# Kernel tuning notes

Hardware: AMD Instinct MI355X
Metric: run time of the kernel (lower is better)

## Reference

```python
import jax, jax.numpy as jnp
import numpy as np

EPS = 1e-6
N_HEADS = 16


def _stable_softmax(x):
    # max subtracted with stop_gradient (torch .detach()), clamp to [-50, 50], eps in denom
    x_max = jax.lax.stop_gradient(jnp.max(x, axis=-1, keepdims=True))
    exp_x = jnp.exp(jnp.clip(x - x_max, -50.0, 50.0))
    return exp_x / (jnp.sum(exp_x, axis=-1, keepdims=True) + EPS)


def setup_inputs() -> dict:
    key = jax.random.key(0)
    k1, k2, k3 = jax.random.split(key, 3)
    B, S, D = 2, 2048, 1024
    x = jax.random.normal(k1, (B, S, D), dtype=jnp.float32)
    Wqkv = jax.random.normal(k2, (3 * D, D), dtype=jnp.float32) * 0.02
    Wout = jax.random.normal(k3, (D, D), dtype=jnp.float32) * (0.02 / np.sqrt(2))
    return {"x": x, "Wqkv": Wqkv, "Wout": Wout}


def reference(x, Wqkv, Wout):
    B, S, D = x.shape
    H = N_HEADS
    Dh = D // H
    scale = 1.0 / np.sqrt(Dh)
    # qkv projection (torch Linear: x @ W.T), split into q,k,v -> (B,H,S,Dh)
    qkv = (x @ Wqkv.T).reshape(B, S, 3, H, Dh)
    qkv = jnp.transpose(qkv, (2, 0, 3, 1, 4))
    q, k, v = qkv[0], qkv[1], qkv[2]
    # chunked attention is mathematically identical to full attention here
    scores = jnp.einsum('bhqd,bhkd->bhqk', q, k) * scale
    attn = _stable_softmax(scores)
    out = jnp.einsum('bhqk,bhkd->bhqd', attn, v)  # (B,H,S,Dh)
    out = jnp.transpose(out, (0, 2, 1, 3)).reshape(B, S, D)
    return out @ Wout.T
```

## Files before the change

### kernel.cpp

```cpp
#include <hip/hip_runtime.h>
#include <hip/hip_bf16.h>
#include <stdint.h>

#define S_LEN   2048
#define D_MODEL 1024
#define NH      16
#define DH      64
#define BATCH   2
#define TOKENS  (BATCH * S_LEN)

typedef __bf16 bf16;
typedef __bf16 bf16x8 __attribute__((ext_vector_type(8)));
typedef __bf16 b16x4  __attribute__((ext_vector_type(4)));
typedef float  f32x4  __attribute__((ext_vector_type(4)));
typedef float  f32x16 __attribute__((ext_vector_type(16)));
typedef unsigned int uint32;

__device__ __forceinline__ void async_lds16(const void* g, void* l) {
  __builtin_amdgcn_global_load_lds((__attribute__((address_space(1))) void*)g,
                                   (__attribute__((address_space(3))) void*)l,
                                   16, 0, 0);
}

#define MFMA16(a, b, c) __builtin_amdgcn_mfma_f32_16x16x32_bf16((a), (b), (c), 0, 0, 0)

__global__ __launch_bounds__(256) void convert2_kernel(
    const float* __restrict__ s0, bf16* __restrict__ d0, int n0,
    const float* __restrict__ s1, bf16* __restrict__ d1, int n1) {
  int i = blockIdx.x * 256 + threadIdx.x;
  const float* s;
  bf16* d;
  if (i < n0) {
    s = s0 + (size_t)i * 8; d = d0 + (size_t)i * 8;
  } else {
    i -= n0;
    if (i >= n1) return;
    s = s1 + (size_t)i * 8; d = d1 + (size_t)i * 8;
  }
  const f32x4 a = *(const f32x4*)s;
  const f32x4 b = *(const f32x4*)(s + 4);
  bf16x8 o;
#pragma unroll
  for (int j = 0; j < 4; j++) { o[j] = (bf16)a[j]; o[j + 4] = (bf16)b[j]; }
  *(bf16x8*)d = o;
}

__global__ __launch_bounds__(512, 2) void gemm_qkv_kernel(
    const bf16* __restrict__ X, const bf16* __restrict__ W,
    bf16* __restrict__ Qo, bf16* __restrict__ Ko, bf16* __restrict__ VTo) {
  extern __shared__ __align__(16) bf16 smem[];
  bf16* const Asb = smem;
  bf16* const Bsb = smem + 32768;

  const int tid  = threadIdx.x;
  const int wave = tid >> 6, lane = tid & 63;
  const int quad = lane >> 4, l16 = lane & 15;
  const int wm = (wave >> 2) * 128;
  const int wn = (wave & 3) * 64;
  const int m0 = blockIdx.y * 256;
  const int n0 = blockIdx.x * 256;

  const int rowc  = tid >> 3;
  const int koffc = ((tid & 7) ^ (rowc & 7)) * 8;
  const bf16* pAlo = X + (size_t)(m0 + rowc) * D_MODEL + koffc;
  const bf16* pAhi = X + (size_t)(m0 + 128 + rowc) * D_MODEL + koffc;
  const bf16* pBlo = W + (size_t)(n0 + rowc) * D_MODEL + koffc;
  const bf16* pBhi = W + (size_t)(n0 + 128 + rowc) * D_MODEL + koffc;
  const int ldc = tid * 8;

  const int swr = l16 & 7;
  const int ko0 = ((0 + quad) ^ swr) * 8;
  const int ko1 = ((4 + quad) ^ swr) * 8;

  f32x4 acc[8][4] = {};
  bf16x8 af[4][2], bfr[4][2];

#define STG(P, LB)                                                        \
  { async_lds16((P), (LB) + ldc);                                         \
    async_lds16((P) + (size_t)64 * D_MODEL, (LB) + ldc + 4096); }

#define BAR()                                                             \
  { asm volatile("" ::: "memory");                                        \
    __builtin_amdgcn_s_barrier();                                         \
    asm volatile("" ::: "memory"); }

  STG(pAlo, Asb)                 pAlo += 64;
  STG(pAhi, Asb + 8192)          pAhi += 64;
  STG(pBlo, Bsb)                 pBlo += 64;
  STG(pBhi, Bsb + 8192)          pBhi += 64;
  STG(pAlo, Asb + 16384)         pAlo += 64;
  STG(pAhi, Asb + 16384 + 8192)  pAhi += 64;
  asm volatile("s_waitcnt vmcnt(4)" ::: "memory");
  __builtin_amdgcn_s_barrier();

#pragma unroll 2
  for (int t = 0; t < 16; t++) {
    const int cur = t & 1;
    const bf16* Ac = Asb + cur * 16384;
    const bf16* Bc = Bsb + cur * 16384;
    bf16* An = Asb + cur * 16384;
    bf16* Bn = Bsb + (cur ^ 1) * 16384;

#pragma unroll
    for (int i = 0; i < 4; i++) {
      af[i][0] = *(const bf16x8*)(Ac + (wm + i * 16 + l16) * 64 + ko0);
      af[i][1] = *(const bf16x8*)(Ac + (wm + i * 16 + l16) * 64 + ko1);
    }
#pragma unroll
    for (int j = 0; j < 2; j++) {
      bfr[j][0] = *(const bf16x8*)(Bc + (wn + j * 16 + l16) * 64 + ko0);
      bfr[j][1] = *(const bf16x8*)(Bc + (wn + j * 16 + l16) * 64 + ko1);
    }
    if (t < 15) { STG(pBlo, Bn) pBlo += 64; }
    BAR();
    __builtin_amdgcn_s_setprio(1);
#pragma unroll
    for (int i = 0; i < 4; i++)
#pragma unroll
      for (int j = 0; j < 2; j++) {
        acc[i][j] = MFMA16(af[i][0], bfr[j][0], acc[i][j]);
        acc[i][j] = MFMA16(af[i][1], bfr[j][1], acc[i][j]);
      }
    __builtin_amdgcn_s_setprio(0);
    BAR();

#pragma unroll
    for (int j = 2; j < 4; j++) {
      bfr[j][0] = *(const bf16x8*)(Bc + (wn + j * 16 + l16) * 64 + ko0);
      bfr[j][1] = *(const bf16x8*)(Bc + (wn + j * 16 + l16) * 64 + ko1);
    }
    if (t < 15) { STG(pBhi, Bn + 8192) pBhi += 64; }
    BAR();
    __builtin_amdgcn_s_setprio(1);
#pragma unroll
    for (int i = 0; i < 4; i++)
#pragma unroll
      for (int j = 2; j < 4; j++) {
        acc[i][j] = MFMA16(af[i][0], bfr[j][0], acc[i][j]);
        acc[i][j] = MFMA16(af[i][1], bfr[j][1], acc[i][j]);
      }
    __builtin_amdgcn_s_setprio(0);
    BAR();

#pragma unroll
    for (int i = 0; i < 4; i++) {
      af[i][0] = *(const bf16x8*)(Ac + (wm + (i + 4) * 16 + l16) * 64 + ko0);
      af[i][1] = *(const bf16x8*)(Ac + (wm + (i + 4) * 16 + l16) * 64 + ko1);
    }
    if (t < 14) { STG(pAlo, An) pAlo += 64; }
    BAR();
    __builtin_amdgcn_s_setprio(1);
#pragma unroll
    for (int i = 0; i < 4; i++)
#pragma unroll
      for (int j = 0; j < 2; j++) {
        acc[i + 4][j] = MFMA16(af[i][0], bfr[j][0], acc[i + 4][j]);
        acc[i + 4][j] = MFMA16(af[i][1], bfr[j][1], acc[i + 4][j]);
      }
    __builtin_amdgcn_s_setprio(0);
    BAR();

    if (t < 14) {
      STG(pAhi, An + 8192) pAhi += 64;
      asm volatile("s_waitcnt vmcnt(4)" ::: "memory");
    } else if (t == 14) {
      asm volatile("s_waitcnt vmcnt(0)" ::: "memory");
    }
    BAR();
    __builtin_amdgcn_s_setprio(1);
#pragma unroll
    for (int i = 0; i < 4; i++)
#pragma unroll
      for (int j = 2; j < 4; j++) {
        acc[i + 4][j] = MFMA16(af[i][0], bfr[j][0], acc[i + 4][j]);
        acc[i + 4][j] = MFMA16(af[i][1], bfr[j][1], acc[i + 4][j]);
      }
    __builtin_amdgcn_s_setprio(0);
    BAR();
  }
#undef STG
#undef BAR

  const int tq = n0 >> 10;
#pragma unroll
  for (int i = 0; i < 8; i++) {
    const int rowb = m0 + wm + i * 16 + quad * 4;
    const int b = rowb >> 11, s0r = rowb & 2047;
#pragma unroll
    for (int j = 0; j < 4; j++) {
      const int col = n0 + wn + j * 16 + l16;
      const int h = (col >> 6) & 15, d = col & 63;
      if (tq == 2) {
        b16x4 v4;
#pragma unroll
        for (int r = 0; r < 4; r++) v4[r] = (bf16)acc[i][j][r];
        *(b16x4*)(VTo + ((size_t)(b * NH + h) * DH + d) * S_LEN + s0r) = v4;
      } else {
#pragma unroll
        for (int r = 0; r < 4; r++) {
          const float v = acc[i][j][r];
          if (tq == 0)
            Qo[((size_t)(b * NH + h) * S_LEN + s0r + r) * DH + d] = (bf16)(v * 0.125f);
          else
            Ko[((size_t)(b * NH + h) * S_LEN + s0r + r) * DH + d] = (bf16)v;
        }
      }
    }
  }
}

#define BK  32
#define BM2 64
#define BN2 128

__global__ __launch_bounds__(256) void gemm_out_kernel(
    const bf16* __restrict__ A, const bf16* __restrict__ W,
    float* __restrict__ Out) {
  __shared__ __align__(16) bf16 As[BM2 * BK];
  __shared__ __align__(16) bf16 Bs[BN2 * BK];
  const int tid  = threadIdx.x;
  const int wave = tid >> 6, lane = tid & 63;
  const int quad = lane >> 4, l16 = lane & 15;
  const int m0 = blockIdx.y * BM2;
  const int n0 = blockIdx.x * BN2;
  const int wm = (wave >> 1) * 32, wn = (wave & 1) * 64;
  f32x4 acc[2][4] = {};
  const int c0 = tid, c1 = tid + 256;
  for (int k0 = 0; k0 < D_MODEL; k0 += BK) {
    async_lds16(A + (size_t)(m0 + (c0 >> 2)) * D_MODEL + k0 + (c0 & 3) * 8,
                As + c0 * 8);
    async_lds16(W + (size_t)(n0 + (c0 >> 2)) * D_MODEL + k0 + (c0 & 3) * 8,
                Bs + c0 * 8);
    async_lds16(W + (size_t)(n0 + (c1 >> 2)) * D_MODEL + k0 + (c1 & 3) * 8,
                Bs + c1 * 8);
    __syncthreads();
    bf16x8 af[2], bfr[4];
#pragma unroll
    for (int i = 0; i < 2; i++)
      af[i] = *(const bf16x8*)(As + (wm + i * 16 + l16) * BK + quad * 8);
#pragma unroll
    for (int j = 0; j < 4; j++)
      bfr[j] = *(const bf16x8*)(Bs + (wn + j * 16 + l16) * BK + quad * 8);
#pragma unroll
    for (int i = 0; i < 2; i++)
#pragma unroll
      for (int j = 0; j < 4; j++)
        acc[i][j] = MFMA16(af[i], bfr[j], acc[i][j]);
    __syncthreads();
  }
#pragma unroll
  for (int i = 0; i < 2; i++) {
    const int rowb = m0 + wm + i * 16 + quad * 4;
#pragma unroll
    for (int j = 0; j < 4; j++) {
      const int col = n0 + wn + j * 16 + l16;
#pragma unroll
      for (int r = 0; r < 4; r++)
        Out[(size_t)(rowb + r) * D_MODEL + col] = acc[i][j][r];
    }
  }
}

__global__ __launch_bounds__(512, 2) void attn_kernel(
    const bf16* __restrict__ Q, const bf16* __restrict__ K,
    const bf16* __restrict__ VT, bf16* __restrict__ AO) {
  __shared__ __align__(16) bf16 smem[2][2][2 * 64 * 64];

  const int tid  = threadIdx.x;
  const int lane = tid & 63;
  const int wave = tid >> 6;
  const int g    = wave >> 2;
  const int qw   = wave & 3;
  const int l31  = lane & 31;
  const int hi   = lane >> 5;
  const int sw   = l31 & 7;

  const int bid = (blockIdx.x & 7) * 32 + (blockIdx.x >> 3);
  const int qb  = bid & 7;
  const int bh  = bid >> 3;

  const bf16* qp = Q  + ((size_t)bh * S_LEN + qb * 256 + qw * 64 + l31) * DH;
  const bf16* kp = K  + (size_t)bh * S_LEN * DH;
  const bf16* vp = VT + (size_t)bh * DH * S_LEN;

  bf16x8 qf0[4], qf1[4];
#pragma unroll
  for (int dk = 0; dk < 4; dk++) {
    qf0[dk] = *(const bf16x8*)(qp + dk * 16 + hi * 8);
    qf1[dk] = *(const bf16x8*)(qp + 32 * DH + dk * 16 + hi * 8);
  }

  const int gtid = tid & 255;
  const int cid0 = gtid, cid1 = gtid + 256;
  const int r0 = cid0 >> 3, c0 = (cid0 & 7) ^ (r0 & 7);
  const int r1 = cid1 >> 3, c1 = (cid1 & 7) ^ (r1 & 7);
  const bf16* ka0 = kp + (size_t)(g * 64 + r0) * DH + c0 * 8;
  const bf16* ka1 = kp + (size_t)(g * 64 + r1) * DH + c1 * 8;
  const bf16* va0 = vp + (size_t)r0 * S_LEN + g * 64 + c0 * 8;
  const bf16* va1 = vp + (size_t)r1 * S_LEN + g * 64 + c1 * 8;
  const int ld0 = cid0 * 8, ld1 = cid1 * 8;

  f32x16 oT0[2] = {}, oT1[2] = {};
  float lsum0 = 0.f, lsum1 = 0.f;

  bf16* sg = &smem[g][0][0];

#define STAGE(B)                                                                 \
  {                                                                              \
    bf16* s = sg + (B) * (2 * 64 * 64);                                          \
    async_lds16(ka0, s + ld0);                                                   \
    async_lds16(ka1, s + ld1);                                                   \
    async_lds16(va0, s + 4096 + ld0);                                            \
    async_lds16(va1, s + 4096 + ld1);                                            \
    ka0 += 8192; ka1 += 8192; va0 += 128; va1 += 128;                            \
  }

  STAGE(0)

#pragma unroll 2
  for (int t = 0; t < 16; t++) {
    const int cur = t & 1;
    asm volatile("s_waitcnt vmcnt(0)" ::: "memory");
    __builtin_amdgcn_s_barrier();
    if (t < 15) {
      STAGE(cur ^ 1)
    }

    const bf16* sb = sg + cur * (2 * 64 * 64);

    bf16x8 vfr[8];
#pragma unroll
    for (int dt = 0; dt < 2; dt++)
#pragma unroll
      for (int ks = 0; ks < 4; ks++)
        vfr[dt * 4 + ks] = *(const bf16x8*)(sb + 4096 + (dt * 32 + l31) * 64 +
                                            (((ks * 2 + hi) ^ sw) * 8));

    f32x16 st0[2] = {}, st1[2] = {};
    __builtin_amdgcn_s_setprio(1);
#pragma unroll
    for (int kt = 0; kt < 2; kt++)
#pragma unroll
      for (int dk = 0; dk < 4; dk++) {
        const bf16x8 kf = *(const bf16x8*)(sb + (kt * 32 + l31) * 64 +
                                           (((dk * 2 + hi) ^ sw) * 8));
        st0[kt] = __builtin_amdgcn_mfma_f32_32x32x16_bf16(kf, qf0[dk], st0[kt], 0, 0, 0);
        st1[kt] = __builtin_amdgcn_mfma_f32_32x32x16_bf16(kf, qf1[dk], st1[kt], 0, 0, 0);
      }
    __builtin_amdgcn_s_setprio(0);

#pragma unroll
    for (int kt = 0; kt < 2; kt++)
#pragma unroll
      for (int hk = 0; hk < 2; hk++) {
        const int ks = kt * 2 + hk;
        float e0[8], e1[8];
#pragma unroll
        for (int r = 0; r < 8; r++) e0[r] = __expf(st0[kt][hk * 8 + r]);
#pragma unroll
        for (int r = 0; r < 8; r++) e1[r] = __expf(st1[kt][hk * 8 + r]);
        lsum0 += ((e0[0] + e0[1]) + (e0[2] + e0[3])) + ((e0[4] + e0[5]) + (e0[6] + e0[7]));
        lsum1 += ((e1[0] + e1[1]) + (e1[2] + e1[3])) + ((e1[4] + e1[5]) + (e1[6] + e1[7]));
        uint32 p00, p01, p02, p03, p10, p11, p12, p13;
        asm("v_cvt_pk_bf16_f32 %0, %1, %2" : "=v"(p00) : "v"(e0[0]), "v"(e0[1]));
        asm("v_cvt_pk_bf16_f32 %0, %1, %2" : "=v"(p01) : "v"(e0[2]), "v"(e0[3]));
        asm("v_cvt_pk_bf16_f32 %0, %1, %2" : "=v"(p02) : "v"(e0[4]), "v"(e0[5]));
        asm("v_cvt_pk_bf16_f32 %0, %1, %2" : "=v"(p03) : "v"(e0[6]), "v"(e0[7]));
        asm("v_cvt_pk_bf16_f32 %0, %1, %2" : "=v"(p10) : "v"(e1[0]), "v"(e1[1]));
        asm("v_cvt_pk_bf16_f32 %0, %1, %2" : "=v"(p11) : "v"(e1[2]), "v"(e1[3]));
        asm("v_cvt_pk_bf16_f32 %0, %1, %2" : "=v"(p12) : "v"(e1[4]), "v"(e1[5]));
        asm("v_cvt_pk_bf16_f32 %0, %1, %2" : "=v"(p13) : "v"(e1[6]), "v"(e1[7]));
        asm("v_permlane32_swap_b32 %0, %1" : "+v"(p00), "+v"(p02));
        asm("v_permlane32_swap_b32 %0, %1" : "+v"(p01), "+v"(p03));
        asm("v_permlane32_swap_b32 %0, %1" : "+v"(p10), "+v"(p12));
        asm("v_permlane32_swap_b32 %0, %1" : "+v"(p11), "+v"(p13));
        union { uint32 u[4]; bf16x8 v; } pf0, pf1;
        pf0.u[0] = p00; pf0.u[1] = p01; pf0.u[2] = p02; pf0.u[3] = p03;
        pf1.u[0] = p10; pf1.u[1] = p11; pf1.u[2] = p12; pf1.u[3] = p13;
        __builtin_amdgcn_s_setprio(1);
#pragma unroll
        for (int dt = 0; dt < 2; dt++) {
          oT0[dt] = __builtin_amdgcn_mfma_f32_32x32x16_bf16(vfr[dt * 4 + ks], pf0.v,
                                                            oT0[dt], 0, 0, 0);
          oT1[dt] = __builtin_amdgcn_mfma_f32_32x32x16_bf16(vfr[dt * 4 + ks], pf1.v,
                                                            oT1[dt], 0, 0, 0);
        }
        __builtin_amdgcn_s_setprio(0);
      }
  }
#undef STAGE

  __syncthreads();

  lsum0 += __shfl_xor(lsum0, 32);
  lsum1 += __shfl_xor(lsum1, 32);

  float* mO = (float*)&smem[0][0][0];
  float* mL = mO + 256 * 32;
  const int mrow = qw * 64 + lane;

  if (g == 1) {
#pragma unroll
    for (int j = 0; j < 8; j++) {
      const int dt = j >> 2, rb = (j & 3) * 4;
      f32x4 c = { oT0[dt][rb], oT0[dt][rb + 1], oT0[dt][rb + 2], oT0[dt][rb + 3] };
      *(f32x4*)((char*)mO + mrow * 128 + ((j ^ (lane & 7)) * 16)) = c;
    }
    mL[mrow] = lsum0;
  }
  __syncthreads();
  if (g == 0) {
#pragma unroll
    for (int j = 0; j < 8; j++) {
      const int dt = j >> 2, rb = (j & 3) * 4;
      const f32x4 c = *(const f32x4*)((char*)mO + mrow * 128 + ((j ^ (lane & 7)) * 16));
#pragma unroll
      for (int rr = 0; rr < 4; rr++) oT0[dt][rb + rr] += c[rr];
    }
    lsum0 += mL[mrow];
  }
  __syncthreads();
  if (g == 1) {
#pragma unroll
    for (int j = 0; j < 8; j++) {
      const int dt = j >> 2, rb = (j & 3) * 4;
      f32x4 c = { oT1[dt][rb], oT1[dt][rb + 1], oT1[dt][rb + 2], oT1[dt][rb + 3] };
      *(f32x4*)((char*)mO + mrow * 128 + ((j ^ (lane & 7)) * 16)) = c;
    }
    mL[mrow] = lsum1;
  }
  __syncthreads();
  if (g == 0) {
#pragma unroll
    for (int j = 0; j < 8; j++) {
      const int dt = j >> 2, rb = (j & 3) * 4;
      const f32x4 c = *(const f32x4*)((char*)mO + mrow * 128 + ((j ^ (lane & 7)) * 16));
#pragma unroll
      for (int rr = 0; rr < 4; rr++) oT1[dt][rb + rr] += c[rr];
    }
    lsum1 += mL[mrow];

    const float inv0 = 1.0f / (lsum0 + 1e-6f);
    const float inv1 = 1.0f / (lsum1 + 1e-6f);
    const int b = bh >> 4, h = bh & 15;
    const int srow = qb * 256 + qw * 64 + l31;
    const size_t base0 = (size_t)(b * S_LEN + srow) * D_MODEL + h * DH;
    const size_t base1 = base0 + (size_t)32 * D_MODEL;
#pragma unroll
    for (int dt = 0; dt < 2; dt++)
#pragma unroll
      for (int rg = 0; rg < 4; rg++) {
        b16x4 o4;
#pragma unroll
        for (int rr = 0; rr < 4; rr++) o4[rr] = (bf16)(oT0[dt][rg * 4 + rr] * inv0);
        *(b16x4*)(AO + base0 + dt * 32 + rg * 8 + hi * 4) = o4;
      }
#pragma unroll
    for (int dt = 0; dt < 2; dt++)
#pragma unroll
      for (int rg = 0; rg < 4; rg++) {
        b16x4 o4;
#pragma unroll
        for (int rr = 0; rr < 4; rr++) o4[rr] = (bf16)(oT1[dt][rg * 4 + rr] * inv1);
        *(b16x4*)(AO + base1 + dt * 32 + rg * 8 + hi * 4) = o4;
      }
  }
}

extern "C" void kernel_launch(void* const* d_in, const int* in_sizes, int n_in,
                              void* d_out, int out_size, void* d_ws, size_t ws_size,
                              hipStream_t stream) {
  const float* x    = (const float*)d_in[0];
  const float* wqkv = (const float*)d_in[1];
  const float* wout = (const float*)d_in[2];
  float* out = (float*)d_out;

  bf16* Q  = (bf16*)d_ws;
  bf16* K  = Q  + (size_t)TOKENS * D_MODEL;
  bf16* VT = K  + (size_t)TOKENS * D_MODEL;
  bf16* xb = VT + (size_t)TOKENS * D_MODEL;
  bf16* AO = xb;
  bf16* wqkvb = (bf16*)d_out;
  bf16* woutb = Q;

  const int nx = TOKENS * D_MODEL / 8;
  const int nw = 3 * D_MODEL * D_MODEL / 8;
  const int no = D_MODEL * D_MODEL / 8;
  convert2_kernel<<<dim3((nx + nw) / 256), dim3(256), 0, stream>>>(
      x, xb, nx, wqkv, wqkvb, nw);

  gemm_qkv_kernel<<<dim3(3 * D_MODEL / 256, TOKENS / 256), dim3(512),
                    131072, stream>>>(xb, wqkvb, Q, K, VT);

  attn_kernel<<<dim3(BATCH * NH * (S_LEN / 256)), dim3(512), 0, stream>>>(Q, K, VT, AO);

  convert2_kernel<<<dim3(no / 256), dim3(256), 0, stream>>>(
      wout, woutb, no, wout, woutb, 0);

  gemm_out_kernel<<<dim3(D_MODEL / BN2, TOKENS / BM2), dim3(256), 0, stream>>>(
      AO, woutb, out);
}
```

Measured before the change: 177.6 us.

## Halve attention query tile to 128 rows per block for more occupancy

The attention kernel now processes 32 query rows per wave instead of 64, so each block covers 128 queries and the grid doubles to 512 blocks. Launch bounds are raised to 4 blocks per CU, and the merge between the two key-split wave groups needs only one LDS round. This cuts per-wave register pressure and increases parallelism. The cost is that K/V tiles are reloaded twice as often per query, and each K/V fragment read from LDS feeds only one MFMA instead of two.

```diff
diff --git a/kernel.cpp b/kernel.cpp
--- a/kernel.cpp
+++ b/kernel.cpp
@@ -261,7 +261,7 @@
   }
 }
 
-__global__ __launch_bounds__(512, 2) void attn_kernel(
+__global__ __launch_bounds__(512, 4) void attn_kernel(
     const bf16* __restrict__ Q, const bf16* __restrict__ K,
     const bf16* __restrict__ VT, bf16* __restrict__ AO) {
   __shared__ __align__(16) bf16 smem[2][2][2 * 64 * 64];
@@ -275,20 +275,18 @@
   const int hi   = lane >> 5;
   const int sw   = l31 & 7;
 
-  const int bid = (blockIdx.x & 7) * 32 + (blockIdx.x >> 3);
-  const int qb  = bid & 7;
-  const int bh  = bid >> 3;
-
-  const bf16* qp = Q  + ((size_t)bh * S_LEN + qb * 256 + qw * 64 + l31) * DH;
+  const int bid = (blockIdx.x & 7) * 64 + (blockIdx.x >> 3);
+  const int qb  = bid & 15;
+  const int bh  = bid >> 4;
+
+  const bf16* qp = Q  + ((size_t)bh * S_LEN + qb * 128 + qw * 32 + l31) * DH;
   const bf16* kp = K  + (size_t)bh * S_LEN * DH;
   const bf16* vp = VT + (size_t)bh * DH * S_LEN;
 
-  bf16x8 qf0[4], qf1[4];
-#pragma unroll
-  for (int dk = 0; dk < 4; dk++) {
-    qf0[dk] = *(const bf16x8*)(qp + dk * 16 + hi * 8);
-    qf1[dk] = *(const bf16x8*)(qp + 32 * DH + dk * 16 + hi * 8);
-  }
+  bf16x8 qf[4];
+#pragma unroll
+  for (int dk = 0; dk < 4; dk++)
+    qf[dk] = *(const bf16x8*)(qp + dk * 16 + hi * 8);
 
   const int gtid = tid & 255;
   const int cid0 = gtid, cid1 = gtid + 256;
@@ -300,8 +298,8 @@
   const bf16* va1 = vp + (size_t)r1 * S_LEN + g * 64 + c1 * 8;
   const int ld0 = cid0 * 8, ld1 = cid1 * 8;
 
-  f32x16 oT0[2] = {}, oT1[2] = {};
-  float lsum0 = 0.f, lsum1 = 0.f;
+  f32x16 oT[2] = {};
+  float lsum = 0.f;
 
   bf16* sg = &smem[g][0][0];
 
@@ -336,7 +334,7 @@
         vfr[dt * 4 + ks] = *(const bf16x8*)(sb + 4096 + (dt * 32 + l31) * 64 +
                                             (((ks * 2 + hi) ^ sw) * 8));
 
-    f32x16 st0[2] = {}, st1[2] = {};
+    f32x16 st[2] = {};
     __builtin_amdgcn_s_setprio(1);
 #pragma unroll
     for (int kt = 0; kt < 2; kt++)
@@ -344,8 +342,7 @@
       for (int dk = 0; dk < 4; dk++) {
         const bf16x8 kf = *(const bf16x8*)(sb + (kt * 32 + l31) * 64 +
                                            (((dk * 2 + hi) ^ sw) * 8));
-        st0[kt] = __builtin_amdgcn_mfma_f32_32x32x16_bf16(kf, qf0[dk], st0[kt], 0, 0, 0);
-        st1[kt] = __builtin_amdgcn_mfma_f32_32x32x16_bf16(kf, qf1[dk], st1[kt], 0, 0, 0);
+        st[kt] = __builtin_amdgcn_mfma_f32_32x32x16_bf16(kf, qf[dk], st[kt], 0, 0, 0);
       }
     __builtin_amdgcn_s_setprio(0);
 
@@ -354,37 +351,24 @@
 #pragma unroll
       for (int hk = 0; hk < 2; hk++) {
         const int ks = kt * 2 + hk;
-        float e0[8], e1[8];
-#pragma unroll
-        for (int r = 0; r < 8; r++) e0[r] = __expf(st0[kt][hk * 8 + r]);
-#pragma unroll
-        for (int r = 0; r < 8; r++) e1[r] = __expf(st1[kt][hk * 8 + r]);
-        lsum0 += ((e0[0] + e0[1]) + (e0[2] + e0[3])) + ((e0[4] + e0[5]) + (e0[6] + e0[7]));
-        lsum1 += ((e1[0] + e1[1]) + (e1[2] + e1[3])) + ((e1[4] + e1[5]) + (e1[6] + e1[7]));
-        uint32 p00, p01, p02, p03, p10, p11, p12, p13;
+        float e0[8];
+#pragma unroll
+        for (int r = 0; r < 8; r++) e0[r] = __expf(st[kt][hk * 8 + r]);
+        lsum += ((e0[0] + e0[1]) + (e0[2] + e0[3])) + ((e0[4] + e0[5]) + (e0[6] + e0[7]));
+        uint32 p00, p01, p02, p03;
         asm("v_cvt_pk_bf16_f32 %0, %1, %2" : "=v"(p00) : "v"(e0[0]), "v"(e0[1]));
         asm("v_cvt_pk_bf16_f32 %0, %1, %2" : "=v"(p01) : "v"(e0[2]), "v"(e0[3]));
         asm("v_cvt_pk_bf16_f32 %0, %1, %2" : "=v"(p02) : "v"(e0[4]), "v"(e0[5]));
         asm("v_cvt_pk_bf16_f32 %0, %1, %2" : "=v"(p03) : "v"(e0[6]), "v"(e0[7]));
-        asm("v_cvt_pk_bf16_f32 %0, %1, %2" : "=v"(p10) : "v"(e1[0]), "v"(e1[1]));
-        asm("v_cvt_pk_bf16_f32 %0, %1, %2" : "=v"(p11) : "v"(e1[2]), "v"(e1[3]));
-        asm("v_cvt_pk_bf16_f32 %0, %1, %2" : "=v"(p12) : "v"(e1[4]), "v"(e1[5]));
-        asm("v_cvt_pk_bf16_f32 %0, %1, %2" : "=v"(p13) : "v"(e1[6]), "v"(e1[7]));
         asm("v_permlane32_swap_b32 %0, %1" : "+v"(p00), "+v"(p02));
         asm("v_permlane32_swap_b32 %0, %1" : "+v"(p01), "+v"(p03));
-        asm("v_permlane32_swap_b32 %0, %1" : "+v"(p10), "+v"(p12));
-        asm("v_permlane32_swap_b32 %0, %1" : "+v"(p11), "+v"(p13));
-        union { uint32 u[4]; bf16x8 v; } pf0, pf1;
-        pf0.u[0] = p00; pf0.u[1] = p01; pf0.u[2] = p02; pf0.u[3] = p03;
-        pf1.u[0] = p10; pf1.u[1] = p11; pf1.u[2] = p12; pf1.u[3] = p13;
+        union { uint32 u[4]; bf16x8 v; } pf;
+        pf.u[0] = p00; pf.u[1] = p01; pf.u[2] = p02; pf.u[3] = p03;
         __builtin_amdgcn_s_setprio(1);
 #pragma unroll
-        for (int dt = 0; dt < 2; dt++) {
-          oT0[dt] = __builtin_amdgcn_mfma_f32_32x32x16_bf16(vfr[dt * 4 + ks], pf0.v,
-                                                            oT0[dt], 0, 0, 0);
-          oT1[dt] = __builtin_amdgcn_mfma_f32_32x32x16_bf16(vfr[dt * 4 + ks], pf1.v,
-                                                            oT1[dt], 0, 0, 0);
-        }
+        for (int dt = 0; dt < 2; dt++)
+          oT[dt] = __builtin_amdgcn_mfma_f32_32x32x16_bf16(vfr[dt * 4 + ks], pf.v,
+                                                           oT[dt], 0, 0, 0);
         __builtin_amdgcn_s_setprio(0);
       }
   }
@@ -392,8 +376,7 @@
 
   __syncthreads();
 
-  lsum0 += __shfl_xor(lsum0, 32);
-  lsum1 += __shfl_xor(lsum1, 32);
+  lsum += __shfl_xor(lsum, 32);
 
   float* mO = (float*)&smem[0][0][0];
   float* mL = mO + 256 * 32;
@@ -403,10 +386,10 @@
 #pragma unroll
     for (int j = 0; j < 8; j++) {
       const int dt = j >> 2, rb = (j & 3) * 4;
-      f32x4 c = { oT0[dt][rb], oT0[dt][rb + 1], oT0[dt][rb + 2], oT0[dt][rb + 3] };
+      f32x4 c = { oT[dt][rb], oT[dt][rb + 1], oT[dt][rb + 2], oT[dt][rb + 3] };
       *(f32x4*)((char*)mO + mrow * 128 + ((j ^ (lane & 7)) * 16)) = c;
     }
-    mL[mrow] = lsum0;
+    mL[mrow] = lsum;
   }
   __syncthreads();
   if (g == 0) {
@@ -415,54 +398,22 @@
       const int dt = j >> 2, rb = (j & 3) * 4;
       const f32x4 c = *(const f32x4*)((char*)mO + mrow * 128 + ((j ^ (lane & 7)) * 16));
 #pragma unroll
-      for (int rr = 0; rr < 4; rr++) oT0[dt][rb + rr] += c[rr];
-    }
-    lsum0 += mL[mrow];
-  }
-  __syncthreads();
-  if (g == 1) {
-#pragma unroll
-    for (int j = 0; j < 8; j++) {
-      const int dt = j >> 2, rb = (j & 3) * 4;
-      f32x4 c = { oT1[dt][rb], oT1[dt][rb + 1], oT1[dt][rb + 2], oT1[dt][rb + 3] };
-      *(f32x4*)((char*)mO + mrow * 128 + ((j ^ (lane & 7)) * 16)) = c;
-    }
-    mL[mrow] = lsum1;
-  }
-  __syncthreads();
-  if (g == 0) {
-#pragma unroll
-    for (int j = 0; j < 8; j++) {
-      const int dt = j >> 2, rb = (j & 3) * 4;
-      const f32x4 c = *(const f32x4*)((char*)mO + mrow * 128 + ((j ^ (lane & 7)) * 16));
-#pragma unroll
-      for (int rr = 0; rr < 4; rr++) oT1[dt][rb + rr] += c[rr];
-    }
-    lsum1 += mL[mrow];
-
-    const float inv0 = 1.0f / (lsum0 + 1e-6f);
-    const float inv1 = 1.0f / (lsum1 + 1e-6f);
+      for (int rr = 0; rr < 4; rr++) oT[dt][rb + rr] += c[rr];
+    }
+    lsum += mL[mrow];
+
+    const float inv = 1.0f / (lsum + 1e-6f);
     const int b = bh >> 4, h = bh & 15;
-    const int srow = qb * 256 + qw * 64 + l31;
-    const size_t base0 = (size_t)(b * S_LEN + srow) * D_MODEL + h * DH;
-    const size_t base1 = base0 + (size_t)32 * D_MODEL;
+    const int srow = qb * 128 + qw * 32 + l31;
+    const size_t base = (size_t)(b * S_LEN + srow) * D_MODEL + h * DH;
 #pragma unroll
     for (int dt = 0; dt < 2; dt++)
 #pragma unroll
       for (int rg = 0; rg < 4; rg++) {
         b16x4 o4;
 #pragma unroll
-        for (int rr = 0; rr < 4; rr++) o4[rr] = (bf16)(oT0[dt][rg * 4 + rr] * inv0);
-        *(b16x4*)(AO + base0 + dt * 32 + rg * 8 + hi * 4) = o4;
-      }
-#pragma unroll
-    for (int dt = 0; dt < 2; dt++)
-#pragma unroll
-      for (int rg = 0; rg < 4; rg++) {
-        b16x4 o4;
-#pragma unroll
-        for (int rr = 0; rr < 4; rr++) o4[rr] = (bf16)(oT1[dt][rg * 4 + rr] * inv1);
-        *(b16x4*)(AO + base1 + dt * 32 + rg * 8 + hi * 4) = o4;
+        for (int rr = 0; rr < 4; rr++) o4[rr] = (bf16)(oT[dt][rg * 4 + rr] * inv);
+        *(b16x4*)(AO + base + dt * 32 + rg * 8 + hi * 4) = o4;
       }
   }
 }
@@ -492,7 +443,7 @@
   gemm_qkv_kernel<<<dim3(3 * D_MODEL / 256, TOKENS / 256), dim3(512),
                     131072, stream>>>(xb, wqkvb, Q, K, VT);
 
-  attn_kernel<<<dim3(BATCH * NH * (S_LEN / 256)), dim3(512), 0, stream>>>(Q, K, VT, AO);
+  attn_kernel<<<dim3(BATCH * NH * (S_LEN / 128)), dim3(512), 0, stream>>>(Q, K, VT, AO);
 
   convert2_kernel<<<dim3(no / 256), dim3(256), 0, stream>>>(
       wout, woutb, no, wout, woutb, 0);
```

New measurement: 226.4 us. 27.5% more time.
